# Optimization experiments

Hardware: AMD Instinct MI355X
Metric: run time of the kernel (lower is better)

The kernel has to match this reference:

```python
import jax, jax.numpy as jnp
import numpy as np

N_POI = 50000
D = 128
E = 400000
GCN_NUM = 3
HEADS = 8
B = 64
L = 100
LEAKY_SLOPE = 0.01
NORM_EPS = 1e-12


def setup_inputs() -> dict:
    key = jax.random.key(0)
    ks = jax.random.split(key, 11)
    return {
        "embeds": jax.random.normal(ks[0], (N_POI, D), jnp.float32) * 0.1,
        "gcn_W": jax.random.normal(ks[1], (GCN_NUM, D, D), jnp.float32) * (1.0 / np.sqrt(D)),
        "gcn_b": jnp.zeros((GCN_NUM, D), jnp.float32),
        "in_proj_w": jax.random.normal(ks[2], (3 * D, D), jnp.float32) * (1.0 / np.sqrt(D)),
        "in_proj_b": jnp.zeros((3 * D,), jnp.float32),
        "out_proj_w": jax.random.normal(ks[3], (D, D), jnp.float32) * (1.0 / np.sqrt(D)),
        "out_proj_b": jnp.zeros((D,), jnp.float32),
        "dist_vec": jax.random.uniform(ks[4], (E,), jnp.float32),
        "dist_edges": jax.random.randint(ks[5], (2, E), 0, N_POI),
        "x_idx": jax.random.randint(ks[6], (B * L,), 0, N_POI),
        "poi_idx": jax.random.randint(ks[7], (B,), 0, N_POI),
    }


def _self_attn(x, in_w, in_b, out_w, out_b):
    # x: [B, L, D]; standard nn.MultiheadAttention with Q=K=V=x, batch_first
    b, l, d = x.shape
    hd = d // HEADS
    qkv = x @ in_w.T + in_b                      # [B, L, 3D]
    q, k, v = jnp.split(qkv, 3, axis=-1)
    def heads(t):
        return t.reshape(b, l, HEADS, hd).transpose(0, 2, 1, 3)  # [B, H, L, hd]
    q, k, v = heads(q), heads(k), heads(v)
    scores = jnp.einsum('bhqd,bhkd->bhqk', q, k) / jnp.sqrt(jnp.asarray(hd, x.dtype))
    attn = jax.nn.softmax(scores, axis=-1)
    o = jnp.einsum('bhqk,bhkd->bhqd', attn, v).transpose(0, 2, 1, 3).reshape(b, l, d)
    return o @ out_w.T + out_b


def reference(embeds, gcn_W, gcn_b, in_proj_w, in_proj_b, out_proj_w, out_proj_b,
              dist_vec, dist_edges, x_idx, poi_idx):
    n_poi = embeds.shape[0]
    loop = jnp.arange(n_poi)
    # symmetrize edges + add self-loops (done in GeoGraph.__init__)
    rows = jnp.concatenate([dist_edges[0], dist_edges[1], loop])
    cols = jnp.concatenate([dist_edges[1], dist_edges[0], loop])
    dv = jnp.concatenate([dist_vec, dist_vec, jnp.zeros((n_poi,), dist_vec.dtype)])
    # symmetric degree normalization over destination (col) index
    deg = jax.ops.segment_sum(jnp.ones_like(dv), cols, num_segments=n_poi)
    dis = jnp.where(deg > 0, jax.lax.rsqrt(jnp.maximum(deg, 1e-12)), 0.0)
    w = jnp.exp(-dv ** 2) * dis[rows] * dis[cols]   # [E_full]

    enc = embeds
    for i in range(GCN_NUM):
        # sparse.mm: out[row] += w * enc[col]
        agg = jax.ops.segment_sum(w[:, None] * enc[cols], rows, num_segments=n_poi)
        enc = agg @ gcn_W[i].T + gcn_b[i]
        enc = jax.nn.leaky_relu(enc, LEAKY_SLOPE)
        enc = enc / jnp.maximum(jnp.linalg.norm(enc, axis=-1, keepdims=True), NORM_EPS)

    tar_embed = enc[poi_idx]                         # [B, D]
    geo_feat = enc[x_idx].reshape(B, L, D)           # equal-length sessions -> pad is a reshape
    attn_out = _self_attn(geo_feat, in_proj_w, in_proj_b, out_proj_w, out_proj_b)
    aggr_feat = attn_out.mean(axis=1)                # [B, D]
    return aggr_feat, tar_embed
```

## Files before the change

### kernel.cpp

```cpp
#include <hip/hip_runtime.h>
#include <math.h>

#define D 128
#define GCN_NUM 3
#define HEADS 8
#define HD 16
#define L_SEQ 100
#define LEAKY 0.01f

typedef __attribute__((ext_vector_type(8))) short short8v;
typedef __attribute__((ext_vector_type(4))) float f32x4;

__device__ __forceinline__ unsigned f2bf(float x) {
  unsigned u = __float_as_uint(x);
  return (u + 0x7FFFu + ((u >> 16) & 1u)) >> 16;
}
__device__ __forceinline__ float bflo2f(unsigned u) {
  return __uint_as_float(u << 16);
}
__device__ __forceinline__ float bfhi2f(unsigned u) {
  return __uint_as_float(u & 0xFFFF0000u);
}


__global__ void f32_to_bf16_kernel(const float* __restrict__ src,
                                   unsigned short* __restrict__ dst, int n4) {
  int i = blockIdx.x * blockDim.x + threadIdx.x;
  if (i < n4) {
    float4 v = reinterpret_cast<const float4*>(src)[i];
    uint2 o;
    o.x = f2bf(v.x) | (f2bf(v.y) << 16);
    o.y = f2bf(v.z) | (f2bf(v.w) << 16);
    reinterpret_cast<uint2*>(dst)[i] = o;
  }
}


__global__ void fill_deg(int* __restrict__ deg, int n) {
  int i = blockIdx.x * blockDim.x + threadIdx.x;
  if (i < n) deg[i] = 1;
}

__global__ void count_deg(const int* __restrict__ e0, const int* __restrict__ e1,
                          int* __restrict__ deg, int E) {
  int stride = gridDim.x * blockDim.x;
  for (int i = blockIdx.x * blockDim.x + threadIdx.x; i < E; i += stride) {
    atomicAdd(&deg[e0[i]], 1);
    atomicAdd(&deg[e1[i]], 1);
  }
}


__global__ __launch_bounds__(1024) void block_sum(const int* __restrict__ deg,
                                                  int* __restrict__ bsum, int n) {
  __shared__ int ws[16];
  int tid = threadIdx.x, lane = tid & 63, wid = tid >> 6;
  int i = blockIdx.x * 1024 + tid;
  int v = (i < n) ? deg[i] : 0;
#pragma unroll
  for (int off = 32; off; off >>= 1) v += __shfl_xor(v, off);
  if (lane == 0) ws[wid] = v;
  __syncthreads();
  if (tid == 0) {
    int s = 0;
#pragma unroll
    for (int k = 0; k < 16; ++k) s += ws[k];
    bsum[blockIdx.x] = s;
  }
}

__global__ void scan_bsum(int* __restrict__ bsum, int* __restrict__ total_out, int nb) {
  int tid = threadIdx.x;
  int v = (tid < nb) ? bsum[tid] : 0;
  int x = v;
#pragma unroll
  for (int off = 1; off < 64; off <<= 1) {
    int y = __shfl_up(x, off);
    if (tid >= off) x += y;
  }
  if (tid < nb) bsum[tid] = x - v;
  if (tid == 63) *total_out = x;
}

__global__ __launch_bounds__(1024) void scan_final(
    const int* __restrict__ deg, const int* __restrict__ bsum,
    int* __restrict__ row_ptr, int* __restrict__ cursor, int n) {
  __shared__ int ws[16];
  int tid = threadIdx.x, lane = tid & 63, wid = tid >> 6;
  int i = blockIdx.x * 1024 + tid;
  int v = (i < n) ? deg[i] : 0;
  int x = v;
#pragma unroll
  for (int off = 1; off < 64; off <<= 1) {
    int y = __shfl_up(x, off);
    if (lane >= off) x += y;
  }
  if (lane == 63) ws[wid] = x;
  __syncthreads();
  if (wid == 0) {
    int s = (lane < 16) ? ws[lane] : 0;
#pragma unroll
    for (int off = 1; off < 16; off <<= 1) {
      int y = __shfl_up(s, off);
      if (lane >= off) s += y;
    }
    if (lane < 16) ws[lane] = s;
  }
  __syncthreads();
  int woff = wid ? ws[wid - 1] : 0;
  if (i < n) {
    int pval = bsum[blockIdx.x] + woff + (x - v);
    row_ptr[i] = pval;
    cursor[i] = pval;
  }
}

__global__ void scatter_edges(const int* __restrict__ e0, const int* __restrict__ e1,
                              const float* __restrict__ dv, const int* __restrict__ deg,
                              int* __restrict__ cursor, uint2* __restrict__ ecw,
                              int E, int N) {
  int total = 2 * E + N;
  int stride = gridDim.x * blockDim.x;
  for (int i = blockIdx.x * blockDim.x + threadIdx.x; i < total; i += stride) {
    int r, c; float d;
    if (i < E)          { r = e0[i];     c = e1[i];     d = dv[i]; }
    else if (i < 2 * E) { r = e1[i - E]; c = e0[i - E]; d = dv[i - E]; }
    else                { r = i - 2 * E; c = r;         d = 0.f; }
    float w = expf(-d * d) * (1.0f / sqrtf((float)deg[r])) * (1.0f / sqrtf((float)deg[c]));
    int pos = atomicAdd(&cursor[r], 1);
    ecw[pos] = make_uint2((unsigned)c, __float_as_uint(w));
  }
}


__global__ __launch_bounds__(256) void spmm_bf(
    const int* __restrict__ row_ptr, const uint2* __restrict__ ecw,
    const unsigned short* __restrict__ enc, unsigned short* __restrict__ agg, int n) {
  int r = blockIdx.x * 4 + (threadIdx.x >> 6);
  if (r >= n) return;
  int lane = threadIdx.x & 63;
  int g = lane >> 4, t = lane & 15;
  int s = row_ptr[r], e = row_ptr[r + 1];
  float a0 = 0.f, a1 = 0.f, a2 = 0.f, a3 = 0.f, a4 = 0.f, a5 = 0.f, a6 = 0.f, a7 = 0.f;
  int i = s + g;
  uint2 cw = make_uint2(0u, 0u);
  if (i < e) cw = ecw[i];
  while (i < e) {
    int c = (int)cw.x;
    float wv = __uint_as_float(cw.y);
    int inx = i + 4;
    uint2 nxt = cw;
    if (inx < e) nxt = ecw[inx];
    uint4 u = *reinterpret_cast<const uint4*>(enc + (size_t)c * D + t * 8);
    a0 = fmaf(wv, bflo2f(u.x), a0); a1 = fmaf(wv, bfhi2f(u.x), a1);
    a2 = fmaf(wv, bflo2f(u.y), a2); a3 = fmaf(wv, bfhi2f(u.y), a3);
    a4 = fmaf(wv, bflo2f(u.z), a4); a5 = fmaf(wv, bfhi2f(u.z), a5);
    a6 = fmaf(wv, bflo2f(u.w), a6); a7 = fmaf(wv, bfhi2f(u.w), a7);
    cw = nxt; i = inx;
  }
  a0 += __shfl_xor(a0, 16); a0 += __shfl_xor(a0, 32);
  a1 += __shfl_xor(a1, 16); a1 += __shfl_xor(a1, 32);
  a2 += __shfl_xor(a2, 16); a2 += __shfl_xor(a2, 32);
  a3 += __shfl_xor(a3, 16); a3 += __shfl_xor(a3, 32);
  a4 += __shfl_xor(a4, 16); a4 += __shfl_xor(a4, 32);
  a5 += __shfl_xor(a5, 16); a5 += __shfl_xor(a5, 32);
  a6 += __shfl_xor(a6, 16); a6 += __shfl_xor(a6, 32);
  a7 += __shfl_xor(a7, 16); a7 += __shfl_xor(a7, 32);
  if (g == 0) {
    uint4 o;
    o.x = f2bf(a0) | (f2bf(a1) << 16);
    o.y = f2bf(a2) | (f2bf(a3) << 16);
    o.z = f2bf(a4) | (f2bf(a5) << 16);
    o.w = f2bf(a6) | (f2bf(a7) << 16);
    *reinterpret_cast<uint4*>(agg + (size_t)r * D + t * 8) = o;
  }
}

__global__ __launch_bounds__(256) void dense_mfma(
    const unsigned short* __restrict__ A,
    const unsigned short* __restrict__ Wb,
    const float* __restrict__ bias,
    unsigned short* __restrict__ enc,
    int n) {
  __shared__ unsigned short Wl[128 * 136];
  int tid = threadIdx.x;
  {
    int cg = (tid & 15) * 8;
    int r0 = tid >> 4;
#pragma unroll
    for (int i = 0; i < 8; ++i) {
      int row = r0 + i * 16;
      *reinterpret_cast<short8v*>(&Wl[row * 136 + cg]) =
          *reinterpret_cast<const short8v*>(Wb + row * D + cg);
    }
  }
  __syncthreads();
  int w = tid >> 6, lane = tid & 63;
  int lr = lane & 15, lg = lane >> 4;
#pragma unroll
  for (int rt = 0; rt < 2; ++rt) {
    int rbase = blockIdx.x * 128 + rt * 64 + w * 16;
    f32x4 acc[8];
#pragma unroll
    for (int j = 0; j < 8; ++j) acc[j] = f32x4{0.f, 0.f, 0.f, 0.f};
    const unsigned short* arow = A + (size_t)(rbase + lr) * D + lg * 8;
#pragma unroll
    for (int ks = 0; ks < 4; ++ks) {
      short8v a = *reinterpret_cast<const short8v*>(arow + ks * 32);
#pragma unroll
      for (int jt = 0; jt < 8; ++jt) {
        short8v b = *reinterpret_cast<const short8v*>(&Wl[(jt * 16 + lr) * 136 + ks * 32 + lg * 8]);
        acc[jt] = __builtin_amdgcn_mfma_f32_16x16x32_bf16(a, b, acc[jt], 0, 0, 0);
      }
    }
    float vals[8][4];
    float ss[4] = {0.f, 0.f, 0.f, 0.f};
#pragma unroll
    for (int jt = 0; jt < 8; ++jt) {
      float bj = bias[jt * 16 + lr];
#pragma unroll
      for (int i = 0; i < 4; ++i) {
        float t = acc[jt][i] + bj;
        t = (t > 0.f) ? t : LEAKY * t;
        vals[jt][i] = t;
        ss[i] += t * t;
      }
    }
#pragma unroll
    for (int i = 0; i < 4; ++i) {
      float s = ss[i];
      s += __shfl_xor(s, 1); s += __shfl_xor(s, 2);
      s += __shfl_xor(s, 4); s += __shfl_xor(s, 8);
      ss[i] = 1.0f / fmaxf(sqrtf(s), 1e-12f);
    }
#pragma unroll
    for (int i = 0; i < 4; ++i) {
      int row = rbase + lg * 4 + i;
      if (row < n) {
#pragma unroll
        for (int jt = 0; jt < 8; ++jt)
          enc[(size_t)row * D + jt * 16 + lr] = (unsigned short)f2bf(vals[jt][i] * ss[i]);
      }
    }
  }
}


__global__ void gather_bf(const unsigned short* __restrict__ src,
                          const int* __restrict__ idx,
                          unsigned short* __restrict__ dst, int M) {
  int i = blockIdx.x;
  if (i < M) {
    int t = threadIdx.x;
    reinterpret_cast<unsigned*>(dst + (size_t)i * D)[t] =
        reinterpret_cast<const unsigned*>(src + (size_t)idx[i] * D)[t];
  }
}

__global__ void gather_bf_to_f32(const unsigned short* __restrict__ src,
                                 const int* __restrict__ idx,
                                 float* __restrict__ dst, int M) {
  int i = blockIdx.x;
  if (i < M) {
    int t = threadIdx.x;
    dst[(size_t)i * D + t] = bflo2f(src[(size_t)idx[i] * D + t]);
  }
}

__global__ __launch_bounds__(256) void qkv_mfma(
    const unsigned short* __restrict__ A,
    const unsigned short* __restrict__ Wb,
    const float* __restrict__ bias,
    float* __restrict__ qkv, int M) {
  __shared__ unsigned short Wl[128 * 136];
  int tid = threadIdx.x;
  const unsigned short* Wslab = Wb + (size_t)blockIdx.y * 128 * D;
  {
    int cg = (tid & 15) * 8;
    int r0 = tid >> 4;
#pragma unroll
    for (int i = 0; i < 8; ++i) {
      int row = r0 + i * 16;
      *reinterpret_cast<short8v*>(&Wl[row * 136 + cg]) =
          *reinterpret_cast<const short8v*>(Wslab + row * D + cg);
    }
  }
  __syncthreads();
  int w = tid >> 6, lane = tid & 63;
  int lr = lane & 15, lg = lane >> 4;
  int colbase = blockIdx.y * 128;
#pragma unroll
  for (int rt = 0; rt < 2; ++rt) {
    int rbase = blockIdx.x * 128 + rt * 64 + w * 16;
    f32x4 acc[8];
#pragma unroll
    for (int j = 0; j < 8; ++j) acc[j] = f32x4{0.f, 0.f, 0.f, 0.f};
    const unsigned short* arow = A + (size_t)(rbase + lr) * D + lg * 8;
#pragma unroll
    for (int ks = 0; ks < 4; ++ks) {
      short8v a = *reinterpret_cast<const short8v*>(arow + ks * 32);
#pragma unroll
      for (int jt = 0; jt < 8; ++jt) {
        short8v b = *reinterpret_cast<const short8v*>(&Wl[(jt * 16 + lr) * 136 + ks * 32 + lg * 8]);
        acc[jt] = __builtin_amdgcn_mfma_f32_16x16x32_bf16(a, b, acc[jt], 0, 0, 0);
      }
    }
#pragma unroll
    for (int jt = 0; jt < 8; ++jt) {
      int j = colbase + jt * 16 + lr;
      float bj = bias[j];
#pragma unroll
      for (int i = 0; i < 4; ++i) {
        int row = rbase + lg * 4 + i;
        if (row < M) qkv[(size_t)row * 384 + j] = acc[jt][i] + bj;
      }
    }
  }
}

__global__ __launch_bounds__(128) void attn_kernel(
    const float* __restrict__ qkv, float* __restrict__ o) {
  __shared__ float k_s[L_SEQ][HD];
  __shared__ float v_s[L_SEQ][HD];
  __shared__ float sc[L_SEQ][L_SEQ + 1];
  int b = blockIdx.x / HEADS;
  int h = blockIdx.x % HEADS;
  int tid = threadIdx.x;
  const size_t rowbase = (size_t)b * L_SEQ;
  for (int idx = tid; idx < L_SEQ * HD; idx += 128) {
    int l = idx >> 4, d2 = idx & 15;
    const float* base = qkv + (rowbase + l) * 384 + h * HD + d2;
    k_s[l][d2] = base[128];
    v_s[l][d2] = base[256];
  }
  __syncthreads();
  if (tid < L_SEQ) {
    float q[HD];
    const float* qp = qkv + (rowbase + tid) * 384 + h * HD;
#pragma unroll
    for (int d2 = 0; d2 < HD; ++d2) q[d2] = qp[d2];
    float m = -1e30f;
    for (int j = 0; j < L_SEQ; ++j) {
      float s = 0.f;
#pragma unroll
      for (int d2 = 0; d2 < HD; ++d2) s += q[d2] * k_s[j][d2];
      s *= 0.25f;
      sc[tid][j] = s;
      m = fmaxf(m, s);
    }
    float sum = 0.f;
    for (int j = 0; j < L_SEQ; ++j) {
      float e = expf(sc[tid][j] - m);
      sc[tid][j] = e;
      sum += e;
    }
    float inv = 1.f / sum;
    float oacc[HD];
#pragma unroll
    for (int d2 = 0; d2 < HD; ++d2) oacc[d2] = 0.f;
    for (int j = 0; j < L_SEQ; ++j) {
      float p = sc[tid][j];
#pragma unroll
      for (int d2 = 0; d2 < HD; ++d2) oacc[d2] += p * v_s[j][d2];
    }
    float* op = o + (rowbase + tid) * D + h * HD;
#pragma unroll
    for (int d2 = 0; d2 < HD; ++d2) op[d2] = oacc[d2] * inv;
  }
}

__global__ __launch_bounds__(128) void out_mean_kernel(
    const float* __restrict__ o, const float* __restrict__ Wo,
    const float* __restrict__ bo, float* __restrict__ out, int L) {
  __shared__ float m_s[D];
  int b = blockIdx.x, tid = threadIdx.x;
  float s = 0.f;
  for (int l = 0; l < L; ++l) s += o[((size_t)b * L + l) * D + tid];
  m_s[tid] = s / (float)L;
  __syncthreads();
  const float4* w4 = reinterpret_cast<const float4*>(Wo + (size_t)tid * D);
  float acc = 0.f;
  for (int k4 = 0; k4 < D / 4; ++k4) {
    float4 w = w4[k4];
    int k = k4 * 4;
    acc += m_s[k] * w.x + m_s[k + 1] * w.y + m_s[k + 2] * w.z + m_s[k + 3] * w.w;
  }
  out[(size_t)b * D + tid] = acc + bo[tid];
}


extern "C" void kernel_launch(void* const* d_in, const int* in_sizes, int n_in,
                              void* d_out, int out_size, void* d_ws, size_t ws_size,
                              hipStream_t stream) {
  const float* embeds   = (const float*)d_in[0];
  const float* gcn_W    = (const float*)d_in[1];
  const float* gcn_b    = (const float*)d_in[2];
  const float* in_w     = (const float*)d_in[3];
  const float* in_b     = (const float*)d_in[4];
  const float* out_w    = (const float*)d_in[5];
  const float* out_b    = (const float*)d_in[6];
  const float* dist_vec = (const float*)d_in[7];
  const int*   edges    = (const int*)d_in[8];
  const int*   x_idx    = (const int*)d_in[9];
  const int*   poi_idx  = (const int*)d_in[10];
  float* out = (float*)d_out;

  int N  = in_sizes[0] / D;
  int E  = in_sizes[7];
  int BL = in_sizes[9];
  int B  = in_sizes[10];
  int L  = BL / B;
  const int* e0 = edges;
  const int* e1 = edges + E;
  size_t total_edges = (size_t)2 * E + N;
  int Npad = ((N + 127) / 128) * 128;
  int NB   = (N + 1023) / 1024;

  char* p = (char*)d_ws;
  auto alloc = [&](size_t bytes) { char* q = p; p += (bytes + 255) & ~(size_t)255; return q; };
  int*   deg     = (int*)alloc((size_t)N * 4);
  int*   row_ptr = (int*)alloc((size_t)(N + 1) * 4);
  int*   cursor  = (int*)alloc((size_t)N * 4);
  int*   bsum    = (int*)alloc((size_t)NB * 4);
  uint2* ecw     = (uint2*)alloc(total_edges * 8);
  unsigned short* emb_bf = (unsigned short*)alloc((size_t)Npad * D * 2);
  unsigned short* W_bf   = (unsigned short*)alloc((size_t)GCN_NUM * D * D * 2);
  unsigned short* inw_bf = (unsigned short*)alloc((size_t)3 * D * D * 2);
  unsigned short* agg_bf = (unsigned short*)alloc((size_t)Npad * D * 2);
  unsigned short* enc_bf = (unsigned short*)alloc((size_t)Npad * D * 2);
  unsigned short* geo_bf = (unsigned short*)alloc((size_t)BL * D * 2);
  float* qkv  = (float*)alloc((size_t)BL * 384 * 4);
  float* obuf = (float*)alloc((size_t)BL * D * 4);

  int n4e = N * D / 4;
  f32_to_bf16_kernel<<<(n4e + 255) / 256, 256, 0, stream>>>(embeds, emb_bf, n4e);
  int n4w = GCN_NUM * D * D / 4;
  f32_to_bf16_kernel<<<(n4w + 255) / 256, 256, 0, stream>>>(gcn_W, W_bf, n4w);
  int n4i = 3 * D * D / 4;
  f32_to_bf16_kernel<<<(n4i + 255) / 256, 256, 0, stream>>>(in_w, inw_bf, n4i);

  fill_deg<<<(N + 255) / 256, 256, 0, stream>>>(deg, N);
  count_deg<<<1024, 256, 0, stream>>>(e0, e1, deg, E);
  block_sum<<<NB, 1024, 0, stream>>>(deg, bsum, N);
  scan_bsum<<<1, 64, 0, stream>>>(bsum, row_ptr + N, NB);
  scan_final<<<NB, 1024, 0, stream>>>(deg, bsum, row_ptr, cursor, N);
  scatter_edges<<<2048, 256, 0, stream>>>(e0, e1, dist_vec, deg, cursor, ecw, E, N);

  const unsigned short* cur_in = emb_bf;
  for (int i = 0; i < GCN_NUM; ++i) {
    spmm_bf<<<(N + 3) / 4, 256, 0, stream>>>(row_ptr, ecw, cur_in, agg_bf, N);
    dense_mfma<<<Npad / 128, 256, 0, stream>>>(
        agg_bf, W_bf + (size_t)i * D * D, gcn_b + (size_t)i * D, enc_bf, N);
    cur_in = enc_bf;
  }

  gather_bf<<<BL, 64, 0, stream>>>(enc_bf, x_idx, geo_bf, BL);
  gather_bf_to_f32<<<B, 128, 0, stream>>>(enc_bf, poi_idx, out + (size_t)B * D, B);
  dim3 qgrid(BL / 128, 3);
  qkv_mfma<<<qgrid, 256, 0, stream>>>(geo_bf, inw_bf, in_b, qkv, BL);
  attn_kernel<<<B * HEADS, 128, 0, stream>>>(qkv, obuf);
  out_mean_kernel<<<B, 128, 0, stream>>>(obuf, out_w, out_b, out, L);
}
```

Before: 380.9 us.

## Merge small kernels, bucket edge scatter by row, and unroll SpMM gather loop

Fuses the three bf16 conversion launches into one, folds the block-sum scan into scan_final, and merges the two gathers into a single launch, all to cut launch overhead. The edge scatter now runs in row buckets, so each block group only writes edges whose rows fall in its range. The aim is better locality for the cursor atomics and ecw writes, at the cost of every bucket re-reading all edges. The SpMM inner loop is unrolled by two, so two neighbour rows are fetched per iteration for more memory-level parallelism.

```diff
diff --git a/kernel.cpp b/kernel.cpp
--- a/kernel.cpp
+++ b/kernel.cpp
@@ -7,6 +7,7 @@
 #define HD 16
 #define L_SEQ 100
 #define LEAKY 0.01f
+#define SC_BUCKETS 8
 
 typedef __attribute__((ext_vector_type(8))) short short8v;
 typedef __attribute__((ext_vector_type(4))) float f32x4;
@@ -15,24 +16,24 @@
   unsigned u = __float_as_uint(x);
   return (u + 0x7FFFu + ((u >> 16) & 1u)) >> 16;
 }
-__device__ __forceinline__ float bflo2f(unsigned u) {
-  return __uint_as_float(u << 16);
-}
-__device__ __forceinline__ float bfhi2f(unsigned u) {
-  return __uint_as_float(u & 0xFFFF0000u);
-}
-
-
-__global__ void f32_to_bf16_kernel(const float* __restrict__ src,
-                                   unsigned short* __restrict__ dst, int n4) {
+__device__ __forceinline__ float bflo2f(unsigned u) { return __uint_as_float(u << 16); }
+__device__ __forceinline__ float bfhi2f(unsigned u) { return __uint_as_float(u & 0xFFFF0000u); }
+
+
+__global__ void convert3(const float* __restrict__ s0, unsigned short* __restrict__ d0, int n0,
+                         const float* __restrict__ s1, unsigned short* __restrict__ d1, int n1,
+                         const float* __restrict__ s2, unsigned short* __restrict__ d2, int n2) {
   int i = blockIdx.x * blockDim.x + threadIdx.x;
-  if (i < n4) {
-    float4 v = reinterpret_cast<const float4*>(src)[i];
-    uint2 o;
-    o.x = f2bf(v.x) | (f2bf(v.y) << 16);
-    o.y = f2bf(v.z) | (f2bf(v.w) << 16);
-    reinterpret_cast<uint2*>(dst)[i] = o;
-  }
+  const float* s; unsigned short* d; int j;
+  if (i < n0)            { s = s0; d = d0; j = i; }
+  else if (i < n0 + n1)  { s = s1; d = d1; j = i - n0; }
+  else if (i < n0 + n1 + n2) { s = s2; d = d2; j = i - n0 - n1; }
+  else return;
+  float4 v = reinterpret_cast<const float4*>(s)[j];
+  uint2 o;
+  o.x = f2bf(v.x) | (f2bf(v.y) << 16);
+  o.y = f2bf(v.z) | (f2bf(v.w) << 16);
+  reinterpret_cast<uint2*>(d)[j] = o;
 }
 
 
@@ -69,23 +70,11 @@
   }
 }
 
-__global__ void scan_bsum(int* __restrict__ bsum, int* __restrict__ total_out, int nb) {
-  int tid = threadIdx.x;
-  int v = (tid < nb) ? bsum[tid] : 0;
-  int x = v;
-#pragma unroll
-  for (int off = 1; off < 64; off <<= 1) {
-    int y = __shfl_up(x, off);
-    if (tid >= off) x += y;
-  }
-  if (tid < nb) bsum[tid] = x - v;
-  if (tid == 63) *total_out = x;
-}
-
 __global__ __launch_bounds__(1024) void scan_final(
     const int* __restrict__ deg, const int* __restrict__ bsum,
-    int* __restrict__ row_ptr, int* __restrict__ cursor, int n) {
+    int* __restrict__ row_ptr, int* __restrict__ cursor, int n, int nb) {
   __shared__ int ws[16];
+  __shared__ int prefix_s;
   int tid = threadIdx.x, lane = tid & 63, wid = tid >> 6;
   int i = blockIdx.x * 1024 + tid;
   int v = (i < n) ? deg[i] : 0;
@@ -98,6 +87,10 @@
   if (lane == 63) ws[wid] = x;
   __syncthreads();
   if (wid == 0) {
+    int pv = (lane < blockIdx.x) ? bsum[lane] : 0;
+#pragma unroll
+    for (int off = 32; off; off >>= 1) pv += __shfl_xor(pv, off);
+    if (lane == 0) prefix_s = pv;
     int s = (lane < 16) ? ws[lane] : 0;
 #pragma unroll
     for (int off = 1; off < 16; off <<= 1) {
@@ -108,24 +101,33 @@
   }
   __syncthreads();
   int woff = wid ? ws[wid - 1] : 0;
+  int prefix = prefix_s;
   if (i < n) {
-    int pval = bsum[blockIdx.x] + woff + (x - v);
+    int pval = prefix + woff + (x - v);
     row_ptr[i] = pval;
     cursor[i] = pval;
   }
-}
-
-__global__ void scatter_edges(const int* __restrict__ e0, const int* __restrict__ e1,
-                              const float* __restrict__ dv, const int* __restrict__ deg,
-                              int* __restrict__ cursor, uint2* __restrict__ ecw,
-                              int E, int N) {
+  if (blockIdx.x == nb - 1 && tid == 0) row_ptr[n] = prefix + ws[15];
+}
+
+__global__ __launch_bounds__(256) void scatter_edges_b(
+    const int* __restrict__ e0, const int* __restrict__ e1,
+    const float* __restrict__ dv, const int* __restrict__ deg,
+    int* __restrict__ cursor, uint2* __restrict__ ecw,
+    int E, int N, int span, int bpb) {
+  int bucket = blockIdx.x / bpb;
+  int bx = blockIdx.x % bpb;
+  int rlo = bucket * span;
+  int rhi = min(rlo + span, N);
   int total = 2 * E + N;
-  int stride = gridDim.x * blockDim.x;
-  for (int i = blockIdx.x * blockDim.x + threadIdx.x; i < total; i += stride) {
-    int r, c; float d;
-    if (i < E)          { r = e0[i];     c = e1[i];     d = dv[i]; }
-    else if (i < 2 * E) { r = e1[i - E]; c = e0[i - E]; d = dv[i - E]; }
-    else                { r = i - 2 * E; c = r;         d = 0.f; }
+  int stride = bpb * 256;
+  for (int i = bx * 256 + threadIdx.x; i < total; i += stride) {
+    int r, c; bool self = false;
+    if (i < E)          { r = e0[i];     c = e1[i]; }
+    else if (i < 2 * E) { r = e1[i - E]; c = e0[i - E]; }
+    else                { r = i - 2 * E; c = r; self = true; }
+    if (r < rlo || r >= rhi) continue;
+    float d = self ? 0.f : dv[(i < E) ? i : i - E];
     float w = expf(-d * d) * (1.0f / sqrtf((float)deg[r])) * (1.0f / sqrtf((float)deg[c]));
     int pos = atomicAdd(&cursor[r], 1);
     ecw[pos] = make_uint2((unsigned)c, __float_as_uint(w));
@@ -143,20 +145,34 @@
   int s = row_ptr[r], e = row_ptr[r + 1];
   float a0 = 0.f, a1 = 0.f, a2 = 0.f, a3 = 0.f, a4 = 0.f, a5 = 0.f, a6 = 0.f, a7 = 0.f;
   int i = s + g;
-  uint2 cw = make_uint2(0u, 0u);
-  if (i < e) cw = ecw[i];
-  while (i < e) {
-    int c = (int)cw.x;
-    float wv = __uint_as_float(cw.y);
-    int inx = i + 4;
-    uint2 nxt = cw;
-    if (inx < e) nxt = ecw[inx];
-    uint4 u = *reinterpret_cast<const uint4*>(enc + (size_t)c * D + t * 8);
-    a0 = fmaf(wv, bflo2f(u.x), a0); a1 = fmaf(wv, bfhi2f(u.x), a1);
-    a2 = fmaf(wv, bflo2f(u.y), a2); a3 = fmaf(wv, bfhi2f(u.y), a3);
-    a4 = fmaf(wv, bflo2f(u.z), a4); a5 = fmaf(wv, bfhi2f(u.z), a5);
-    a6 = fmaf(wv, bflo2f(u.w), a6); a7 = fmaf(wv, bfhi2f(u.w), a7);
-    cw = nxt; i = inx;
+  uint2 cwA = make_uint2(0u, 0u), cwB = make_uint2(0u, 0u);
+  if (i < e) cwA = ecw[i];
+  if (i + 4 < e) cwB = ecw[i + 4];
+  while (i + 4 < e) {
+    uint2 cwC = cwA, cwD = cwB;
+    if (i + 8 < e)  cwC = ecw[i + 8];
+    if (i + 12 < e) cwD = ecw[i + 12];
+    float wA = __uint_as_float(cwA.y), wB = __uint_as_float(cwB.y);
+    uint4 uA = *reinterpret_cast<const uint4*>(enc + (size_t)cwA.x * D + t * 8);
+    uint4 uB = *reinterpret_cast<const uint4*>(enc + (size_t)cwB.x * D + t * 8);
+    a0 = fmaf(wA, bflo2f(uA.x), a0); a1 = fmaf(wA, bfhi2f(uA.x), a1);
+    a2 = fmaf(wA, bflo2f(uA.y), a2); a3 = fmaf(wA, bfhi2f(uA.y), a3);
+    a4 = fmaf(wA, bflo2f(uA.z), a4); a5 = fmaf(wA, bfhi2f(uA.z), a5);
+    a6 = fmaf(wA, bflo2f(uA.w), a6); a7 = fmaf(wA, bfhi2f(uA.w), a7);
+    a0 = fmaf(wB, bflo2f(uB.x), a0); a1 = fmaf(wB, bfhi2f(uB.x), a1);
+    a2 = fmaf(wB, bflo2f(uB.y), a2); a3 = fmaf(wB, bfhi2f(uB.y), a3);
+    a4 = fmaf(wB, bflo2f(uB.z), a4); a5 = fmaf(wB, bfhi2f(uB.z), a5);
+    a6 = fmaf(wB, bflo2f(uB.w), a6); a7 = fmaf(wB, bfhi2f(uB.w), a7);
+    cwA = cwC; cwB = cwD;
+    i += 8;
+  }
+  if (i < e) {
+    float wA = __uint_as_float(cwA.y);
+    uint4 uA = *reinterpret_cast<const uint4*>(enc + (size_t)cwA.x * D + t * 8);
+    a0 = fmaf(wA, bflo2f(uA.x), a0); a1 = fmaf(wA, bfhi2f(uA.x), a1);
+    a2 = fmaf(wA, bflo2f(uA.y), a2); a3 = fmaf(wA, bfhi2f(uA.y), a3);
+    a4 = fmaf(wA, bflo2f(uA.z), a4); a5 = fmaf(wA, bfhi2f(uA.z), a5);
+    a6 = fmaf(wA, bflo2f(uA.w), a6); a7 = fmaf(wA, bfhi2f(uA.w), a7);
   }
   a0 += __shfl_xor(a0, 16); a0 += __shfl_xor(a0, 32);
   a1 += __shfl_xor(a1, 16); a1 += __shfl_xor(a1, 32);
@@ -177,11 +193,8 @@
 }
 
 __global__ __launch_bounds__(256) void dense_mfma(
-    const unsigned short* __restrict__ A,
-    const unsigned short* __restrict__ Wb,
-    const float* __restrict__ bias,
-    unsigned short* __restrict__ enc,
-    int n) {
+    const unsigned short* __restrict__ A, const unsigned short* __restrict__ Wb,
+    const float* __restrict__ bias, unsigned short* __restrict__ enc, int n) {
   __shared__ unsigned short Wl[128 * 136];
   int tid = threadIdx.x;
   {
@@ -246,32 +259,25 @@
 }
 
 
-__global__ void gather_bf(const unsigned short* __restrict__ src,
-                          const int* __restrict__ idx,
-                          unsigned short* __restrict__ dst, int M) {
+__global__ void gather_all(const unsigned short* __restrict__ src,
+                           const int* __restrict__ x_idx, const int* __restrict__ poi_idx,
+                           unsigned short* __restrict__ geo, float* __restrict__ tar,
+                           int BL, int B) {
   int i = blockIdx.x;
-  if (i < M) {
-    int t = threadIdx.x;
-    reinterpret_cast<unsigned*>(dst + (size_t)i * D)[t] =
-        reinterpret_cast<const unsigned*>(src + (size_t)idx[i] * D)[t];
-  }
-}
-
-__global__ void gather_bf_to_f32(const unsigned short* __restrict__ src,
-                                 const int* __restrict__ idx,
-                                 float* __restrict__ dst, int M) {
-  int i = blockIdx.x;
-  if (i < M) {
-    int t = threadIdx.x;
-    dst[(size_t)i * D + t] = bflo2f(src[(size_t)idx[i] * D + t]);
+  int t = threadIdx.x;
+  if (i < BL) {
+    reinterpret_cast<unsigned*>(geo + (size_t)i * D)[t] =
+        reinterpret_cast<const unsigned*>(src + (size_t)x_idx[i] * D)[t];
+  } else {
+    int j = i - BL;
+    unsigned u = reinterpret_cast<const unsigned*>(src + (size_t)poi_idx[j] * D)[t];
+    reinterpret_cast<float2*>(tar + (size_t)j * D)[t] = make_float2(bflo2f(u), bfhi2f(u));
   }
 }
 
 __global__ __launch_bounds__(256) void qkv_mfma(
-    const unsigned short* __restrict__ A,
-    const unsigned short* __restrict__ Wb,
-    const float* __restrict__ bias,
-    float* __restrict__ qkv, int M) {
+    const unsigned short* __restrict__ A, const unsigned short* __restrict__ Wb,
+    const float* __restrict__ bias, float* __restrict__ qkv, int M) {
   __shared__ unsigned short Wl[128 * 136];
   int tid = threadIdx.x;
   const unsigned short* Wslab = Wb + (size_t)blockIdx.y * 128 * D;
@@ -432,19 +438,19 @@
   float* qkv  = (float*)alloc((size_t)BL * 384 * 4);
   float* obuf = (float*)alloc((size_t)BL * D * 4);
 
-  int n4e = N * D / 4;
-  f32_to_bf16_kernel<<<(n4e + 255) / 256, 256, 0, stream>>>(embeds, emb_bf, n4e);
-  int n4w = GCN_NUM * D * D / 4;
-  f32_to_bf16_kernel<<<(n4w + 255) / 256, 256, 0, stream>>>(gcn_W, W_bf, n4w);
-  int n4i = 3 * D * D / 4;
-  f32_to_bf16_kernel<<<(n4i + 255) / 256, 256, 0, stream>>>(in_w, inw_bf, n4i);
+  int n4e = N * D / 4, n4w = GCN_NUM * D * D / 4, n4i = 3 * D * D / 4;
+  int n4tot = n4e + n4w + n4i;
+  convert3<<<(n4tot + 255) / 256, 256, 0, stream>>>(
+      embeds, emb_bf, n4e, gcn_W, W_bf, n4w, in_w, inw_bf, n4i);
 
   fill_deg<<<(N + 255) / 256, 256, 0, stream>>>(deg, N);
   count_deg<<<1024, 256, 0, stream>>>(e0, e1, deg, E);
   block_sum<<<NB, 1024, 0, stream>>>(deg, bsum, N);
-  scan_bsum<<<1, 64, 0, stream>>>(bsum, row_ptr + N, NB);
-  scan_final<<<NB, 1024, 0, stream>>>(deg, bsum, row_ptr, cursor, N);
-  scatter_edges<<<2048, 256, 0, stream>>>(e0, e1, dist_vec, deg, cursor, ecw, E, N);
+  scan_final<<<NB, 1024, 0, stream>>>(deg, bsum, row_ptr, cursor, N, NB);
+  int span = (N + SC_BUCKETS - 1) / SC_BUCKETS;
+  int bpb = 512;
+  scatter_edges_b<<<SC_BUCKETS * bpb, 256, 0, stream>>>(
+      e0, e1, dist_vec, deg, cursor, ecw, E, N, span, bpb);
 
   const unsigned short* cur_in = emb_bf;
   for (int i = 0; i < GCN_NUM; ++i) {
@@ -454,8 +460,8 @@
     cur_in = enc_bf;
   }
 
-  gather_bf<<<BL, 64, 0, stream>>>(enc_bf, x_idx, geo_bf, BL);
-  gather_bf_to_f32<<<B, 128, 0, stream>>>(enc_bf, poi_idx, out + (size_t)B * D, B);
+  gather_all<<<BL + B, 64, 0, stream>>>(enc_bf, x_idx, poi_idx, geo_bf,
+                                        out + (size_t)B * D, BL, B);
   dim3 qgrid(BL / 128, 3);
   qkv_mfma<<<qgrid, 256, 0, stream>>>(geo_bf, inw_bf, in_b, qkv, BL);
   attn_kernel<<<B * HEADS, 128, 0, stream>>>(qkv, obuf);
```

Result: faster. 370.1 us (-2.8%).
